# Optimization experiments

Measured on AMD Instinct MI355X. Metric: run time of the kernel, lower is better.

## Reference

```python
import jax, jax.numpy as jnp
import numpy as np

D_NODE = 256
D_PAIR = 128
C = 32
H = 8
LN_EPS = 1e-5


def layer_norm(x, g, b):
    m = jnp.mean(x, axis=-1, keepdims=True)
    v = jnp.mean(jnp.square(x - m), axis=-1, keepdims=True)
    return (x - m) * jax.lax.rsqrt(v + LN_EPS) * g + b


def self_attention(x, mask, wq, wk, wv, wg, bg, wo, bo=None, bias=None):
    # x: [B, S, R, d], mask: [B, S, R]
    B, S, R, _ = x.shape
    scale = 1.0 / np.sqrt(C)
    q = (jnp.einsum('bsrd,ed->bsre', x, wq) * scale).reshape(B, S, R, H, C)
    k = jnp.einsum('bsrd,ed->bsre', x, wk).reshape(B, S, R, H, C)
    v = jnp.einsum('bsrd,ed->bsre', x, wv).reshape(B, S, R, H, C)
    logits = jnp.einsum('bsqhc,bskhc->bshqk', q, k)
    logits = logits + (1e9 * (mask - 1.0))[:, :, None, None, :]
    if bias is not None:
        logits = logits + bias[:, None]  # [B,1,H,R,R]
    a = jax.nn.softmax(logits, axis=-1)
    o = jnp.einsum('bshqk,bskhc->bsqhc', a, v).reshape(B, S, R, H * C)
    g = jax.nn.sigmoid(jnp.einsum('bsrd,ed->bsre', x, wg) + bg)
    out = jnp.einsum('bsre,de->bsrd', o * g, wo)
    if bo is not None:
        out = out + bo
    return out


def setup_inputs() -> dict:
    key = jax.random.key(0)
    ks = jax.random.split(key, 24)
    B, S, R = 1, 128, 256
    d, dp, hc, dff = D_NODE, D_PAIR, H * C, 4 * D_NODE
    std = 0.02
    inp = {
        'node': jax.random.normal(ks[0], (B, S, R, d), jnp.float32),
        'pair': jax.random.normal(ks[1], (B, R, R, dp), jnp.float32),
        'node_mask': jnp.ones((B, S, R), jnp.float32),
        # row attention (pair-biased)
        'row_ln_m_g': jnp.ones((d,), jnp.float32),
        'row_ln_m_b': jnp.zeros((d,), jnp.float32),
        'row_ln_z_g': jnp.ones((dp,), jnp.float32),
        'row_ln_z_b': jnp.zeros((dp,), jnp.float32),
        'row_b_w': jax.random.normal(ks[2], (H, dp), jnp.float32) / np.sqrt(dp),
        'row_wq': jax.random.normal(ks[3], (hc, d), jnp.float32) * std,
        'row_wk': jax.random.normal(ks[4], (hc, d), jnp.float32) * std,
        'row_wv': jax.random.normal(ks[5], (hc, d), jnp.float32) * std,
        'row_wg': jax.random.normal(ks[6], (hc, d), jnp.float32) * std,
        'row_bg': jnp.ones((hc,), jnp.float32),
        'row_wo': jax.random.normal(ks[7], (d, hc), jnp.float32) * std,
        'row_out_bias': jnp.zeros((d,), jnp.float32),
        # column attention
        'col_ln_g': jnp.ones((d,), jnp.float32),
        'col_ln_b': jnp.zeros((d,), jnp.float32),
        'col_wq': jax.random.normal(ks[8], (hc, d), jnp.float32) * std,
        'col_wk': jax.random.normal(ks[9], (hc, d), jnp.float32) * std,
        'col_wv': jax.random.normal(ks[10], (hc, d), jnp.float32) * std,
        'col_wg': jax.random.normal(ks[11], (hc, d), jnp.float32) * std,
        'col_bg': jnp.ones((hc,), jnp.float32),
        'col_wo': jax.random.normal(ks[12], (d, hc), jnp.float32) * std,
        'col_bo': jnp.zeros((d,), jnp.float32),
        # transition
        'tr_ln_g': jnp.ones((d,), jnp.float32),
        'tr_ln_b': jnp.zeros((d,), jnp.float32),
        'tr_w1': jax.random.normal(ks[13], (dff, d), jnp.float32) * std,
        'tr_b1': jnp.zeros((dff,), jnp.float32),
        'tr_w2': jax.random.normal(ks[14], (d, dff), jnp.float32) * std,
        'tr_b2': jnp.zeros((d,), jnp.float32),
    }
    return inp


def reference(node, pair, node_mask,
              row_ln_m_g, row_ln_m_b, row_ln_z_g, row_ln_z_b, row_b_w,
              row_wq, row_wk, row_wv, row_wg, row_bg, row_wo, row_out_bias,
              col_ln_g, col_ln_b, col_wq, col_wk, col_wv, col_wg, col_bg,
              col_wo, col_bo, tr_ln_g, tr_ln_b, tr_w1, tr_b1, tr_w2, tr_b2):
    # --- MSA row attention with pair bias ---
    M = layer_norm(node, row_ln_m_g, row_ln_m_b)
    Z = layer_norm(pair, row_ln_z_g, row_ln_z_b)
    b = jnp.einsum('bqkd,hd->bhqk', Z, row_b_w)  # pair bias [B,H,R,R]
    attn = self_attention(M, node_mask, row_wq, row_wk, row_wv,
                          row_wg, row_bg, row_wo, bo=None, bias=b)
    # bias_dropout_add in eval mode: residual + attn + fused out bias
    node = node + attn + row_out_bias
    # --- MSA column attention ---
    Mt = jnp.swapaxes(node, 1, 2)            # [B,R,S,d]
    Mn = layer_norm(Mt, col_ln_g, col_ln_b)
    mask_t = jnp.swapaxes(node_mask, 1, 2)   # [B,R,S]
    attn_c = self_attention(Mn, mask_t, col_wq, col_wk, col_wv,
                            col_wg, col_bg, col_wo, bo=col_bo)
    node = node + jnp.swapaxes(attn_c, 1, 2)
    # --- MSA transition ---
    t = layer_norm(node, tr_ln_g, tr_ln_b)
    t = jax.nn.relu(jnp.einsum('bsrd,ed->bsre', t, tr_w1) + tr_b1)
    node = node + (jnp.einsum('bsre,de->bsrd', t, tr_w2) + tr_b2)
    return node
```

## Files before the change

kernel.cpp:

```cpp
#include <hip/hip_runtime.h>
#include <math.h>

#define S 128
#define R 256
#define DMODEL 256
#define H 8
#define CDIM 32
#define HC 256
#define DFF 1024
#define NROWS (S*R)
#define NPAIR (R*R)
#define LN_EPS 1e-5f
#define LOG2E 1.4426950408889634f
#define M32 ((size_t)NROWS * 32)

typedef unsigned short u16;
typedef __attribute__((ext_vector_type(8))) short bf16x8;
typedef __attribute__((ext_vector_type(4))) float f32x4;
typedef __attribute__((ext_vector_type(16))) float f32x16;

__device__ __forceinline__ u16 f2bf(float x) {
  unsigned u = __float_as_uint(x);
  u = (u + 0x7fffu + ((u >> 16) & 1u)) >> 16;
  return (u16)u;
}
__device__ __forceinline__ float bf2f(u16 x) {
  return __uint_as_float(((unsigned)x) << 16);
}
__device__ __forceinline__ unsigned cvt_pk(float a, float b) {
  unsigned r;
  asm("v_cvt_pk_bf16_f32 %0, %1, %2" : "=v"(r) : "v"(a), "v"(b));
  return r;
}
__device__ __forceinline__ void pl32swap(unsigned &a, unsigned &b) {
  asm("v_permlane32_swap_b32 %0, %1" : "+v"(a), "+v"(b));
}
__device__ __forceinline__ bf16x8 mk_frag(unsigned a, unsigned b, unsigned c, unsigned d) {
  uint4 t = make_uint4(a, b, c, d);
  return __builtin_bit_cast(bf16x8, t);
}

__device__ __forceinline__ void gload_lds16(const u16* g, u16* l) {
  __builtin_amdgcn_global_load_lds(
      (const __attribute__((address_space(1))) unsigned int*)g,
      (__attribute__((address_space(3))) unsigned int*)l, 16, 0, 0);
}

struct CvtArgs {
  const float* src[12];
  int off[12];
  int n[12];
  float scale[12];
};

__global__ __launch_bounds__(256) void cvt_w_kernel(CvtArgs a, u16* __restrict__ dst) {
  int sg = blockIdx.y;
  int i = (blockIdx.x * 256 + threadIdx.x) * 4;
  if (i >= a.n[sg]) return;
  float4 v = *(const float4*)(a.src[sg] + i);
  float sc = a.scale[sg];
  uint2 o;
  o.x = cvt_pk(v.x * sc, v.y * sc);
  o.y = cvt_pk(v.z * sc, v.w * sc);
  *(uint2*)(dst + a.off[sg] + i) = o;
}

__global__ __launch_bounds__(256) void ln256_kernel(
    const void* __restrict__ in, u16* __restrict__ out,
    const float* __restrict__ gamma, const float* __restrict__ beta,
    int tmode, int inbf)
{
  int wid = threadIdx.x >> 6, lane = threadIdx.x & 63;
  int m = blockIdx.x * 4 + wid;
  int inrow = m;
  if (tmode) { int r = m >> 7, s = m & 127; inrow = s * R + r; }
  float4 x;
  if (inbf) {
    ushort4 u = *(const ushort4*)((const u16*)in + (size_t)inrow * DMODEL + lane * 4);
    x.x = bf2f(u.x); x.y = bf2f(u.y); x.z = bf2f(u.z); x.w = bf2f(u.w);
  } else {
    x = *(const float4*)((const float*)in + (size_t)inrow * DMODEL + lane * 4);
  }
  float sum = x.x + x.y + x.z + x.w;
  float sq  = x.x*x.x + x.y*x.y + x.z*x.z + x.w*x.w;
  #pragma unroll
  for (int off = 32; off; off >>= 1) {
    sum += __shfl_xor(sum, off);
    sq  += __shfl_xor(sq, off);
  }
  float mean = sum * (1.0f/256.0f);
  float var  = sq  * (1.0f/256.0f) - mean*mean;
  float rstd = rsqrtf(var + LN_EPS);
  float4 g = *(const float4*)(gamma + lane*4);
  float4 b = *(const float4*)(beta  + lane*4);
  uint2 o;
  o.x = cvt_pk((x.x-mean)*rstd*g.x + b.x, (x.y-mean)*rstd*g.y + b.y);
  o.y = cvt_pk((x.z-mean)*rstd*g.z + b.z, (x.w-mean)*rstd*g.w + b.w);
  *(uint2*)(out + (size_t)m * DMODEL + lane*4) = o;
}

__global__ __launch_bounds__(256) void pair_bias_kernel(
    const float* __restrict__ pair, const float* __restrict__ gamma,
    const float* __restrict__ beta, const float* __restrict__ bw,
    u16* __restrict__ bias)
{
  int wid = threadIdx.x >> 6, lane = threadIdx.x & 63;
  int p = blockIdx.x * 4 + wid;
  float2 x = *(const float2*)(pair + (size_t)p * 128 + lane*2);
  float sum = x.x + x.y, sq = x.x*x.x + x.y*x.y;
  #pragma unroll
  for (int off = 32; off; off >>= 1) {
    sum += __shfl_xor(sum, off);
    sq  += __shfl_xor(sq, off);
  }
  float mean = sum * (1.0f/128.0f);
  float rstd = rsqrtf(sq*(1.0f/128.0f) - mean*mean + LN_EPS);
  float z0 = (x.x-mean)*rstd*gamma[lane*2]   + beta[lane*2];
  float z1 = (x.y-mean)*rstd*gamma[lane*2+1] + beta[lane*2+1];
  float a0 = z0*bw[0*128+lane*2] + z1*bw[0*128+lane*2+1];
  float a1 = z0*bw[1*128+lane*2] + z1*bw[1*128+lane*2+1];
  float a2 = z0*bw[2*128+lane*2] + z1*bw[2*128+lane*2+1];
  float a3 = z0*bw[3*128+lane*2] + z1*bw[3*128+lane*2+1];
  float a4 = z0*bw[4*128+lane*2] + z1*bw[4*128+lane*2+1];
  float a5 = z0*bw[5*128+lane*2] + z1*bw[5*128+lane*2+1];
  float a6 = z0*bw[6*128+lane*2] + z1*bw[6*128+lane*2+1];
  float a7 = z0*bw[7*128+lane*2] + z1*bw[7*128+lane*2+1];
  #pragma unroll
  for (int off = 32; off; off >>= 1) {
    a0 += __shfl_xor(a0, off); a1 += __shfl_xor(a1, off);
    a2 += __shfl_xor(a2, off); a3 += __shfl_xor(a3, off);
    a4 += __shfl_xor(a4, off); a5 += __shfl_xor(a5, off);
    a6 += __shfl_xor(a6, off); a7 += __shfl_xor(a7, off);
  }
  float v = a0;
  v = (lane==1)?a1:v; v = (lane==2)?a2:v; v = (lane==3)?a3:v;
  v = (lane==4)?a4:v; v = (lane==5)?a5:v; v = (lane==6)?a6:v; v = (lane==7)?a7:v;
  if (lane < 8) {
    int q = p >> 8, k = p & 255;
    int kt = k >> 5, qt = q >> 5, c31 = q & 31;
    int kk = k & 31;
    int hi2 = (kk >> 2) & 1;
    int j = (kk & 3) | ((kk >> 3) << 2);
    size_t addr = ((((size_t)lane*8 + kt)*8 + qt)*2 + hi2)*512 + (size_t)c31*16 + j;
    bias[addr] = f2bf(v * LOG2E);
  }
}

template<int AM>
__global__ __launch_bounds__(512, 2) void gemm_8ph(
    const u16* __restrict__ A, const u16* __restrict__ W,
    void* __restrict__ Cout, int N, int K,
    int mode, const float* __restrict__ bias, const float* __restrict__ res)
{
  __shared__ u16 lds[2][AM+2][128*64];
  int t = threadIdx.x, lane = t & 63, wv = t >> 6;
  int g16 = (lane >> 4) & 3, l16 = lane & 15;
  int wm = wv >> 2, wn = wv & 3;
  int lrow = lane >> 3, lchunk = lane & 7;

  int gx = gridDim.x;
  int nwg = gx * gridDim.y;
  int p = blockIdx.y * gx + blockIdx.x;
  int cpx = nwg >> 3;
  int lg = (p & 7) * cpx + (p >> 3);
  int bn = (lg % gx) * 256;
  int bm = (lg / gx) * (AM * 128);

  int srcc = (lchunk ^ lrow) << 3;
  int ch0  = (g16 ^ (l16 & 7)) << 3;
  int rdoff = l16 * 64 + ch0;
  const int wnh = AM + (wn >> 1);
  const int wnr = (wn & 1) * 4096;

  f32x4 acc[AM*4][4];
  #pragma unroll
  for (int i = 0; i < AM*4; ++i)
    #pragma unroll
    for (int j = 0; j < 4; ++j) acc[i][j] = (f32x4){0.f,0.f,0.f,0.f};

  const int nkt = K >> 6;

#define STG_HALF(buf_, h_, base_, row0_, kc_) do { \
    gload_lds16(base_ + (size_t)((row0_) + (wv*2+0)*8 + lrow) * K + (kc_) + srcc, \
                &lds[buf_][h_][(wv*2+0)*512 + lane*8]); \
    gload_lds16(base_ + (size_t)((row0_) + (wv*2+1)*8 + lrow) * K + (kc_) + srcc, \
                &lds[buf_][h_][(wv*2+1)*512 + lane*8]); \
  } while(0)
#define STG_A(buf_, kc_) do { STG_HALF(buf_,0,A,bm,kc_); \
    if (AM==2) STG_HALF(buf_,1,A,bm+128,kc_); } while(0)
#define STG_B(buf_, kc_) do { STG_HALF(buf_,AM,W,bn,kc_); STG_HALF(buf_,AM+1,W,bn+128,kc_); } while(0)

  int buf = 0;
  STG_A(0, 0); STG_B(0, 0);
  for (int kt = 0; kt < nkt; ++kt) {
    int kc = kt << 6;
    if (kt + 1 < nkt) {
      STG_A(buf^1, kc + 64);
      if (AM == 2) asm volatile("s_waitcnt vmcnt(4)" ::: "memory");
      else         asm volatile("s_waitcnt vmcnt(2)" ::: "memory");
    } else {
      asm volatile("s_waitcnt vmcnt(0)" ::: "memory");
    }
    __builtin_amdgcn_s_barrier();
    asm volatile("" ::: "memory");
    if (kt + 1 < nkt) STG_B(buf^1, kc + 64);

    const u16* Abase = (AM==2) ? &lds[buf][wm][0] : &lds[buf][0][wm*4096];
    const u16* Wbase = &lds[buf][wnh][wnr];
    bf16x8 wf[4][2];
    #pragma unroll
    for (int nf = 0; nf < 4; ++nf) {
      wf[nf][0] = *(const bf16x8*)(Wbase + nf*1024 + rdoff);
      wf[nf][1] = *(const bf16x8*)(Wbase + nf*1024 + (rdoff ^ 32));
    }
    __builtin_amdgcn_s_setprio(1);
    #pragma unroll
    for (int mf = 0; mf < AM*4; ++mf) {
      bf16x8 a0 = *(const bf16x8*)(Abase + mf*1024 + rdoff);
      bf16x8 a1 = *(const bf16x8*)(Abase + mf*1024 + (rdoff ^ 32));
      #pragma unroll
      for (int nf = 0; nf < 4; ++nf) {
        acc[mf][nf] = __builtin_amdgcn_mfma_f32_16x16x32_bf16(wf[nf][0], a0, acc[mf][nf], 0, 0, 0);
        acc[mf][nf] = __builtin_amdgcn_mfma_f32_16x16x32_bf16(wf[nf][1], a1, acc[mf][nf], 0, 0, 0);
      }
    }
    __builtin_amdgcn_s_setprio(0);
    asm volatile("" ::: "memory");
    __builtin_amdgcn_s_barrier();
    buf ^= 1;
  }
#undef STG_A
#undef STG_B
#undef STG_HALF

  const u16* resb = (const u16*)res;
  int rowb = bm + wm*(AM*64) + l16;
  int colb = bn + wn*64 + (g16 << 2);
  #pragma unroll
  for (int mf = 0; mf < AM*4; ++mf) {
    int row = rowb + mf*16;
    #pragma unroll
    for (int nf = 0; nf < 4; ++nf) {
      int col0 = colb + nf*16;
      f32x4 v = acc[mf][nf];
      if (mode == 6) {
        if (col0 >= 768) {
          float4 b4 = *(const float4*)(bias + col0 - 768);
          v[0] = 1.0f/(1.0f+__expf(-(v[0]+b4.x)));
          v[1] = 1.0f/(1.0f+__expf(-(v[1]+b4.y)));
          v[2] = 1.0f/(1.0f+__expf(-(v[2]+b4.z)));
          v[3] = 1.0f/(1.0f+__expf(-(v[3]+b4.w)));
        }
        uint2 o; o.x = cvt_pk(v[0], v[1]); o.y = cvt_pk(v[2], v[3]);
        size_t i2 = (size_t)(col0 >> 5) * M32 + (size_t)row*32 + (col0 & 31);
        *(uint2*)((u16*)Cout + i2) = o;
      } else if (mode == 3) {
        float4 b4 = *(const float4*)(bias + col0);
        uint2 o;
        o.x = cvt_pk(fmaxf(v[0]+b4.x, 0.f), fmaxf(v[1]+b4.y, 0.f));
        o.y = cvt_pk(fmaxf(v[2]+b4.z, 0.f), fmaxf(v[3]+b4.w, 0.f));
        *(uint2*)((u16*)Cout + (size_t)row*N + col0) = o;
      } else if (mode == 4) {
        size_t i2 = (size_t)row*N + col0;
        float4 r4 = *(const float4*)(res + i2);
        float4 b4 = *(const float4*)(bias + col0);
        float4 o = make_float4(v[0]+r4.x+b4.x, v[1]+r4.y+b4.y,
                               v[2]+r4.z+b4.z, v[3]+r4.w+b4.w);
        *(float4*)((float*)Cout + i2) = o;
      } else if (mode == 5) {
        int rr = row >> 7, ss = row & 127;
        size_t i2 = ((size_t)ss*R + rr)*(size_t)N + col0;
        float4 r4 = *(const float4*)(res + i2);
        float4 b4 = *(const float4*)(bias + col0);
        float4 o = make_float4(v[0]+r4.x+b4.x, v[1]+r4.y+b4.y,
                               v[2]+r4.z+b4.z, v[3]+r4.w+b4.w);
        *(float4*)((float*)Cout + i2) = o;
      } else if (mode == 7) {
        size_t i2 = (size_t)row*N + col0;
        float4 r4 = *(const float4*)(res + i2);
        float4 b4 = *(const float4*)(bias + col0);
        uint2 o;
        o.x = cvt_pk(v[0]+r4.x+b4.x, v[1]+r4.y+b4.y);
        o.y = cvt_pk(v[2]+r4.z+b4.z, v[3]+r4.w+b4.w);
        *(uint2*)((u16*)Cout + i2) = o;
      } else if (mode == 8) {
        int rr = row >> 7, ss = row & 127;
        size_t i2 = ((size_t)ss*R + rr)*(size_t)N + col0;
        ushort4 r4 = *(const ushort4*)(resb + i2);
        float4 b4 = *(const float4*)(bias + col0);
        uint2 o;
        o.x = cvt_pk(v[0]+bf2f(r4.x)+b4.x, v[1]+bf2f(r4.y)+b4.y);
        o.y = cvt_pk(v[2]+bf2f(r4.z)+b4.z, v[3]+bf2f(r4.w)+b4.w);
        *(uint2*)((u16*)Cout + i2) = o;
      } else if (mode == 9) {
        size_t i2 = (size_t)row*N + col0;
        ushort4 r4 = *(const ushort4*)(resb + i2);
        float4 b4 = *(const float4*)(bias + col0);
        float4 o = make_float4(v[0]+bf2f(r4.x)+b4.x, v[1]+bf2f(r4.y)+b4.y,
                               v[2]+bf2f(r4.z)+b4.z, v[3]+bf2f(r4.w)+b4.w);
        *(float4*)((float*)Cout + i2) = o;
      } else if (mode == 2) {
        float4 b4 = *(const float4*)(bias + col0);
        uint2 o;
        o.x = cvt_pk(1.0f/(1.0f+__expf(-(v[0]+b4.x))),
                     1.0f/(1.0f+__expf(-(v[1]+b4.y))));
        o.y = cvt_pk(1.0f/(1.0f+__expf(-(v[2]+b4.z))),
                     1.0f/(1.0f+__expf(-(v[3]+b4.w))));
        *(uint2*)((u16*)Cout + (size_t)row*N + col0) = o;
      } else {
        uint2 o; o.x = cvt_pk(v[0], v[1]); o.y = cvt_pk(v[2], v[3]);
        *(uint2*)((u16*)Cout + (size_t)row*N + col0) = o;
      }
    }
  }
}

template<bool RM>
__device__ __forceinline__ void softmax_pack(
    const f32x16 &sac, const float* __restrict__ lmbp,
    bf16x8 bf0, bf16x8 bf1, int kb, int hi,
    float &lsum, bf16x8 &pf0, bf16x8 &pf1)
{
  float p[16];
  #pragma unroll
  for (int rq = 0; rq < 4; ++rq) {
    int k0 = kb + 8*rq + 4*hi;
    float4 lm4 = *(const float4*)&lmbp[k0];
    float b0 = lm4.x, b1 = lm4.y, b2 = lm4.z, b3 = lm4.w;
    if (RM) {
      if (rq < 2) {
        b0 += bf2f((u16)bf0[4*rq+0]); b1 += bf2f((u16)bf0[4*rq+1]);
        b2 += bf2f((u16)bf0[4*rq+2]); b3 += bf2f((u16)bf0[4*rq+3]);
      } else {
        b0 += bf2f((u16)bf1[4*rq-8+0]); b1 += bf2f((u16)bf1[4*rq-8+1]);
        b2 += bf2f((u16)bf1[4*rq-8+2]); b3 += bf2f((u16)bf1[4*rq-8+3]);
      }
    }
    p[4*rq+0] = exp2f(sac[4*rq+0] + b0);
    p[4*rq+1] = exp2f(sac[4*rq+1] + b1);
    p[4*rq+2] = exp2f(sac[4*rq+2] + b2);
    p[4*rq+3] = exp2f(sac[4*rq+3] + b3);
    lsum += (p[4*rq+0] + p[4*rq+1]) + (p[4*rq+2] + p[4*rq+3]);
  }
  unsigned u0 = cvt_pk(p[0],  p[1]),  u1 = cvt_pk(p[2],  p[3]);
  unsigned u2 = cvt_pk(p[4],  p[5]),  u3 = cvt_pk(p[6],  p[7]);
  unsigned u4 = cvt_pk(p[8],  p[9]),  u5 = cvt_pk(p[10], p[11]);
  unsigned u6 = cvt_pk(p[12], p[13]), u7 = cvt_pk(p[14], p[15]);
  pl32swap(u0, u2); pl32swap(u1, u3);
  pl32swap(u4, u6); pl32swap(u5, u7);
  pf0 = mk_frag(u0, u1, u2, u3);
  pf1 = mk_frag(u4, u5, u6, u7);
}

template<int NKEY, int HPB, bool ROWMODE>
__global__ __launch_bounds__(512, 2) void attn_mfma(
    const u16* __restrict__ QKVG, const u16* __restrict__ biasF,
    const float* __restrict__ mask, u16* __restrict__ og)
{
  __shared__ __align__(16) u16 Vt[HPB][32][NKEY + 8];
  __shared__ float lmb[NKEY];
  constexpr int NKV = NKEY / 32;
  constexpr int WPH = 8 / HPB;
  int b = blockIdx.y;
  int t = threadIdx.x, lane = t & 63, w = t >> 6;
  int c31 = lane & 31, hi = lane >> 5;
  int lh = w / WPH, wtile = w % WPH;
  int hh = blockIdx.x * HPB + lh;

  size_t rbase = (size_t)b * NKEY * 32;
  const u16* Qp = QKVG + (size_t)hh * M32 + rbase;
  const u16* Kp = QKVG + (size_t)(8 + hh) * M32 + rbase;
  const u16* Gp = QKVG + (size_t)(24 + hh) * M32 + rbase;

  for (int i = t; i < HPB*NKEY*4; i += 512) {
    int c0 = (i & 3) * 8;
    int key = (i >> 2) & (NKEY - 1);
    int sh = (i >> 2) / NKEY;
    const u16* Vs = QKVG + (size_t)(16 + blockIdx.x*HPB + sh) * M32 + rbase;
    bf16x8 v8 = *(const bf16x8*)(Vs + (size_t)key*32 + c0);
    #pragma unroll
    for (int j = 0; j < 8; ++j) Vt[sh][c0+j][key] = (u16)v8[j];
  }
  for (int i = t; i < NKEY; i += 512)
    lmb[i] = 1.4426950e9f * ((ROWMODE ? mask[b*R + i] : mask[i*R + b]) - 1.0f);
  __syncthreads();

  int qA = wtile*64 + c31, qB = qA + 32;
  int qtA = wtile*2, qtB = wtile*2 + 1;
  bf16x8 qfA0 = *(const bf16x8*)(Qp + (size_t)qA*32 + hi*8);
  bf16x8 qfA1 = *(const bf16x8*)(Qp + (size_t)qA*32 + 16 + hi*8);
  bf16x8 qfB0 = *(const bf16x8*)(Qp + (size_t)qB*32 + hi*8);
  bf16x8 qfB1 = *(const bf16x8*)(Qp + (size_t)qB*32 + 16 + hi*8);

  f32x16 oA = (f32x16)(0.0f), oB = (f32x16)(0.0f);
  float lsA = 0.f, lsB = 0.f;

#define LOADK(d0_, d1_, g_) do { \
    const u16* kr_ = Kp + ((size_t)((g_)*32) + c31)*32 + hi*8; \
    d0_ = *(const bf16x8*)kr_; d1_ = *(const bf16x8*)(kr_ + 16); \
  } while(0)

#define GROUP_BODY(g_, k0_, k1_) do { \
    int kb_ = (g_) * 32; \
    bf16x8 bA0{}, bA1{}, bB0{}, bB1{}; \
    if (ROWMODE) { \
      const u16* bpA_ = biasF + ((((size_t)hh*8 + (g_))*8 + qtA)*2 + hi)*512 + (size_t)c31*16; \
      bA0 = *(const bf16x8*)bpA_; bA1 = *(const bf16x8*)(bpA_ + 8); \
    } \
    __builtin_amdgcn_s_setprio(1); \
    f32x16 sacA_ = __builtin_amdgcn_mfma_f32_32x32x16_bf16(k0_, qfA0, (f32x16)(0.0f), 0, 0, 0); \
    sacA_ = __builtin_amdgcn_mfma_f32_32x32x16_bf16(k1_, qfA1, sacA_, 0, 0, 0); \
    __builtin_amdgcn_s_setprio(0); \
    bf16x8 va0_ = *(const bf16x8*)&Vt[lh][c31][kb_ + hi*8]; \
    bf16x8 va1_ = *(const bf16x8*)&Vt[lh][c31][kb_ + 16 + hi*8]; \
    bf16x8 pf0_, pf1_; \
    softmax_pack<ROWMODE>(sacA_, lmb, bA0, bA1, kb_, hi, lsA, pf0_, pf1_); \
    __builtin_amdgcn_s_setprio(1); \
    oA = __builtin_amdgcn_mfma_f32_32x32x16_bf16(va0_, pf0_, oA, 0, 0, 0); \
    oA = __builtin_amdgcn_mfma_f32_32x32x16_bf16(va1_, pf1_, oA, 0, 0, 0); \
    __builtin_amdgcn_s_setprio(0); \
    if (ROWMODE) { \
      const u16* bpB_ = biasF + ((((size_t)hh*8 + (g_))*8 + qtB)*2 + hi)*512 + (size_t)c31*16; \
      bB0 = *(const bf16x8*)bpB_; bB1 = *(const bf16x8*)(bpB_ + 8); \
    } \
    __builtin_amdgcn_s_setprio(1); \
    f32x16 sacB_ = __builtin_amdgcn_mfma_f32_32x32x16_bf16(k0_, qfB0, (f32x16)(0.0f), 0, 0, 0); \
    sacB_ = __builtin_amdgcn_mfma_f32_32x32x16_bf16(k1_, qfB1, sacB_, 0, 0, 0); \
    __builtin_amdgcn_s_setprio(0); \
    softmax_pack<ROWMODE>(sacB_, lmb, bB0, bB1, kb_, hi, lsB, pf0_, pf1_); \
    __builtin_amdgcn_s_setprio(1); \
    oB = __builtin_amdgcn_mfma_f32_32x32x16_bf16(va0_, pf0_, oB, 0, 0, 0); \
    oB = __builtin_amdgcn_mfma_f32_32x32x16_bf16(va1_, pf1_, oB, 0, 0, 0); \
    __builtin_amdgcn_s_setprio(0); \
  } while(0)

  bf16x8 ke0{}, ke1{}, ko0{}, ko1{};
  LOADK(ke0, ke1, 0);
  LOADK(ko0, ko1, 1);
  for (int g = 0; g < NKV; g += 2) {
    bf16x8 c0 = ke0, c1 = ke1;
    if (g + 2 < NKV) LOADK(ke0, ke1, g + 2);
    GROUP_BODY(g, c0, c1);
    bf16x8 d0 = ko0, d1 = ko1;
    if (g + 3 < NKV) LOADK(ko0, ko1, g + 3);
    GROUP_BODY(g + 1, d0, d1);
  }
#undef GROUP_BODY
#undef LOADK

  lsA += __shfl_xor(lsA, 32);
  lsB += __shfl_xor(lsB, 32);
  float invA = 1.0f / lsA, invB = 1.0f / lsB;

  size_t baseO = (size_t)b * NKEY * 256 + (size_t)hh * 32;
  #pragma unroll
  for (int tile = 0; tile < 2; ++tile) {
    int q = (tile == 0) ? qA : qB;
    float inv = (tile == 0) ? invA : invB;
    const f32x16 &oo = (tile == 0) ? oA : oB;
    u16* op = og + baseO + (size_t)q * 256;
    const u16* gp = Gp + (size_t)q * 32;
    #pragma unroll
    for (int rq = 0; rq < 4; ++rq) {
      int c0 = 8*rq + 4*hi;
      ushort4 g4 = *(const ushort4*)(gp + c0);
      float f0 = oo[4*rq+0] * inv * bf2f(g4.x);
      float f1 = oo[4*rq+1] * inv * bf2f(g4.y);
      float f2 = oo[4*rq+2] * inv * bf2f(g4.z);
      float f3 = oo[4*rq+3] * inv * bf2f(g4.w);
      uint2 o2; o2.x = cvt_pk(f0, f1); o2.y = cvt_pk(f2, f3);
      *(uint2*)(op + c0) = o2;
    }
  }
}

extern "C" void kernel_launch(void* const* d_in, const int* in_sizes, int n_in,
                              void* d_out, int out_size, void* d_ws, size_t ws_size,
                              hipStream_t stream)
{
  const float* node         = (const float*)d_in[0];
  const float* pair         = (const float*)d_in[1];
  const float* node_mask    = (const float*)d_in[2];
  const float* row_ln_m_g   = (const float*)d_in[3];
  const float* row_ln_m_b   = (const float*)d_in[4];
  const float* row_ln_z_g   = (const float*)d_in[5];
  const float* row_ln_z_b   = (const float*)d_in[6];
  const float* row_b_w      = (const float*)d_in[7];
  const float* row_wq       = (const float*)d_in[8];
  const float* row_wk       = (const float*)d_in[9];
  const float* row_wv       = (const float*)d_in[10];
  const float* row_wg       = (const float*)d_in[11];
  const float* row_bg       = (const float*)d_in[12];
  const float* row_wo       = (const float*)d_in[13];
  const float* row_out_bias = (const float*)d_in[14];
  const float* col_ln_g     = (const float*)d_in[15];
  const float* col_ln_b     = (const float*)d_in[16];
  const float* col_wq       = (const float*)d_in[17];
  const float* col_wk       = (const float*)d_in[18];
  const float* col_wv       = (const float*)d_in[19];
  const float* col_wg       = (const float*)d_in[20];
  const float* col_bg       = (const float*)d_in[21];
  const float* col_wo       = (const float*)d_in[22];
  const float* col_bo       = (const float*)d_in[23];
  const float* tr_ln_g      = (const float*)d_in[24];
  const float* tr_ln_b      = (const float*)d_in[25];
  const float* tr_w1        = (const float*)d_in[26];
  const float* tr_b1        = (const float*)d_in[27];
  const float* tr_w2        = (const float*)d_in[28];
  const float* tr_b2        = (const float*)d_in[29];

  float* out = (float*)d_out;
  char* ws8 = (char*)d_ws;
  const size_t MB = 1ull << 20;
  u16*   A     = (u16*)(ws8);
  u16*   QKVG  = (u16*)(ws8 + 16*MB);
  u16*   Ob    = (u16*)(ws8 + 80*MB);
  u16*   DbF   = (u16*)(ws8 + 96*MB);
  u16*   N1    = (u16*)(ws8 + 100*MB);
  u16*   N2    = (u16*)(ws8 + 116*MB);
  u16*   Wb    = (u16*)(ws8 + 132*MB);
  u16*   T1    = QKVG;

  const float qs = 0.17677669529663687f;

  u16* Wrqkvg = Wb + 0;
  u16* Wro    = Wb + 262144;
  u16* Wcqkvg = Wb + 327680;
  u16* Wco    = Wb + 589824;
  u16* W1w    = Wb + 655360;
  u16* W2w    = Wb + 917504;

  CvtArgs ca;
  const float* srcs[12] = {row_wq,row_wk,row_wv,row_wg,row_wo,
                           col_wq,col_wk,col_wv,col_wg,col_wo,tr_w1,tr_w2};
  int offs[12] = {0,65536,131072,196608,262144,327680,393216,458752,524288,589824,655360,917504};
  int ns[12]   = {65536,65536,65536,65536,65536,65536,65536,65536,65536,65536,262144,262144};
  for (int i = 0; i < 12; ++i) {
    ca.src[i] = srcs[i]; ca.off[i] = offs[i]; ca.n[i] = ns[i];
    ca.scale[i] = (i == 0 || i == 5) ? qs * LOG2E : 1.0f;
  }
  cvt_w_kernel<<<dim3(256,12), 256, 0, stream>>>(ca, Wb);

  dim3 gq(4, 128);
  dim3 go(1, 256);

  ln256_kernel<<<8192, 256, 0, stream>>>(node, A, row_ln_m_g, row_ln_m_b, 0, 0);
  pair_bias_kernel<<<16384, 256, 0, stream>>>(pair, row_ln_z_g, row_ln_z_b, row_b_w, DbF);
  gemm_8ph<2><<<gq, 512, 0, stream>>>(A, Wrqkvg, QKVG, 1024, 256, 6, row_bg, nullptr);
  attn_mfma<256,2,true><<<dim3(4,128), 512, 0, stream>>>(QKVG, DbF, node_mask, Ob);
  gemm_8ph<1><<<go, 512, 0, stream>>>(Ob, Wro, N1, 256, 256, 7, row_out_bias, node);

  ln256_kernel<<<8192, 256, 0, stream>>>(N1, A, col_ln_g, col_ln_b, 1, 1);
  gemm_8ph<2><<<gq, 512, 0, stream>>>(A, Wcqkvg, QKVG, 1024, 256, 6, col_bg, nullptr);
  attn_mfma<128,4,false><<<dim3(2,256), 512, 0, stream>>>(QKVG, nullptr, node_mask, Ob);
  gemm_8ph<1><<<go, 512, 0, stream>>>(Ob, Wco, N2, 256, 256, 8, col_bo, (const float*)N1);

  ln256_kernel<<<8192, 256, 0, stream>>>(N2, A, tr_ln_g, tr_ln_b, 0, 1);
  gemm_8ph<2><<<gq, 512, 0, stream>>>(A, W1w, T1, 1024, 256, 3, tr_b1, nullptr);
  gemm_8ph<1><<<go, 512, 0, stream>>>(T1, W2w, out, 256, 1024, 9, tr_b2, (const float*)N2);
}
```

Measured before the change: 345.8 us.

## Switch GEMM to triple-buffered K=32 LDS pipeline with prefetch depth two

Rewrites the GEMM main loop to use three LDS buffers of 32-wide K tiles instead of two 64-wide tiles, issuing global-to-LDS loads two iterations ahead. The aim is to hide global load latency better and reduce LDS footprint per stage, possibly improving occupancy. In exchange it doubles the number of loop iterations and barriers per K, and changes the swizzle pattern, which could add bank conflicts or overhead.

```diff
diff --git a/kernel.cpp b/kernel.cpp
--- a/kernel.cpp
+++ b/kernel.cpp
@@ -152,11 +152,10 @@
     void* __restrict__ Cout, int N, int K,
     int mode, const float* __restrict__ bias, const float* __restrict__ res)
 {
-  __shared__ u16 lds[2][AM+2][128*64];
+  __shared__ u16 lds[3][AM+2][128*32];
   int t = threadIdx.x, lane = t & 63, wv = t >> 6;
   int g16 = (lane >> 4) & 3, l16 = lane & 15;
   int wm = wv >> 2, wn = wv & 3;
-  int lrow = lane >> 3, lchunk = lane & 7;
 
   int gx = gridDim.x;
   int nwg = gx * gridDim.y;
@@ -166,11 +165,12 @@
   int bn = (lg % gx) * 256;
   int bm = (lg / gx) * (AM * 128);
 
-  int srcc = (lchunk ^ lrow) << 3;
-  int ch0  = (g16 ^ (l16 & 7)) << 3;
-  int rdoff = l16 * 64 + ch0;
+  int sr = t >> 2;
+  int swz8 = ((t & 3) ^ ((sr >> 1) & 3)) << 3;
+  int rdch = (g16 ^ ((l16 >> 1) & 3)) << 3;
+  int rdoff = l16 * 32 + rdch;
   const int wnh = AM + (wn >> 1);
-  const int wnr = (wn & 1) * 4096;
+  const int wnr = (wn & 1) * 2048;
 
   f32x4 acc[AM*4][4];
   #pragma unroll
@@ -178,60 +178,50 @@
     #pragma unroll
     for (int j = 0; j < 4; ++j) acc[i][j] = (f32x4){0.f,0.f,0.f,0.f};
 
-  const int nkt = K >> 6;
-
-#define STG_HALF(buf_, h_, base_, row0_, kc_) do { \
-    gload_lds16(base_ + (size_t)((row0_) + (wv*2+0)*8 + lrow) * K + (kc_) + srcc, \
-                &lds[buf_][h_][(wv*2+0)*512 + lane*8]); \
-    gload_lds16(base_ + (size_t)((row0_) + (wv*2+1)*8 + lrow) * K + (kc_) + srcc, \
-                &lds[buf_][h_][(wv*2+1)*512 + lane*8]); \
+  const int nkt = K >> 5;
+
+#define STAGE(buf_, kc_) do { \
+    gload_lds16(A + (size_t)(bm + sr) * K + (kc_) + swz8, &lds[buf_][0][t*8]); \
+    if (AM == 2) \
+      gload_lds16(A + (size_t)(bm + 128 + sr) * K + (kc_) + swz8, &lds[buf_][1][t*8]); \
+    gload_lds16(W + (size_t)(bn + sr) * K + (kc_) + swz8, &lds[buf_][AM][t*8]); \
+    gload_lds16(W + (size_t)(bn + 128 + sr) * K + (kc_) + swz8, &lds[buf_][AM+1][t*8]); \
   } while(0)
-#define STG_A(buf_, kc_) do { STG_HALF(buf_,0,A,bm,kc_); \
-    if (AM==2) STG_HALF(buf_,1,A,bm+128,kc_); } while(0)
-#define STG_B(buf_, kc_) do { STG_HALF(buf_,AM,W,bn,kc_); STG_HALF(buf_,AM+1,W,bn+128,kc_); } while(0)
-
-  int buf = 0;
-  STG_A(0, 0); STG_B(0, 0);
+
+  STAGE(0, 0);
+  STAGE(1, 32);
   for (int kt = 0; kt < nkt; ++kt) {
-    int kc = kt << 6;
-    if (kt + 1 < nkt) {
-      STG_A(buf^1, kc + 64);
+    if (kt + 2 < nkt) {
+      STAGE((kt + 2) % 3, (kt + 2) * 32);
+      if (AM == 2) asm volatile("s_waitcnt vmcnt(8)" ::: "memory");
+      else         asm volatile("s_waitcnt vmcnt(6)" ::: "memory");
+    } else if (kt + 1 < nkt) {
       if (AM == 2) asm volatile("s_waitcnt vmcnt(4)" ::: "memory");
-      else         asm volatile("s_waitcnt vmcnt(2)" ::: "memory");
+      else         asm volatile("s_waitcnt vmcnt(3)" ::: "memory");
     } else {
       asm volatile("s_waitcnt vmcnt(0)" ::: "memory");
     }
     __builtin_amdgcn_s_barrier();
-    asm volatile("" ::: "memory");
-    if (kt + 1 < nkt) STG_B(buf^1, kc + 64);
-
-    const u16* Abase = (AM==2) ? &lds[buf][wm][0] : &lds[buf][0][wm*4096];
+    int buf = kt % 3;
+    const u16* Abase = (AM == 2) ? &lds[buf][wm][0] : &lds[buf][0][wm*2048];
     const u16* Wbase = &lds[buf][wnh][wnr];
-    bf16x8 wf[4][2];
+    bf16x8 wf[4];
     #pragma unroll
-    for (int nf = 0; nf < 4; ++nf) {
-      wf[nf][0] = *(const bf16x8*)(Wbase + nf*1024 + rdoff);
-      wf[nf][1] = *(const bf16x8*)(Wbase + nf*1024 + (rdoff ^ 32));
-    }
+    for (int nf = 0; nf < 4; ++nf)
+      wf[nf] = *(const bf16x8*)(Wbase + nf*512 + rdoff);
     __builtin_amdgcn_s_setprio(1);
     #pragma unroll
     for (int mf = 0; mf < AM*4; ++mf) {
-      bf16x8 a0 = *(const bf16x8*)(Abase + mf*1024 + rdoff);
-      bf16x8 a1 = *(const bf16x8*)(Abase + mf*1024 + (rdoff ^ 32));
+      bf16x8 a0 = *(const bf16x8*)(Abase + mf*512 + rdoff);
       #pragma unroll
-      for (int nf = 0; nf < 4; ++nf) {
-        acc[mf][nf] = __builtin_amdgcn_mfma_f32_16x16x32_bf16(wf[nf][0], a0, acc[mf][nf], 0, 0, 0);
-        acc[mf][nf] = __builtin_amdgcn_mfma_f32_16x16x32_bf16(wf[nf][1], a1, acc[mf][nf], 0, 0, 0);
-      }
+      for (int nf = 0; nf < 4; ++nf)
+        acc[mf][nf] = __builtin_amdgcn_mfma_f32_16x16x32_bf16(wf[nf], a0, acc[mf][nf], 0, 0, 0);
     }
     __builtin_amdgcn_s_setprio(0);
     asm volatile("" ::: "memory");
     __builtin_amdgcn_s_barrier();
-    buf ^= 1;
-  }
-#undef STG_A
-#undef STG_B
-#undef STG_HALF
+  }
+#undef STAGE
 
   const u16* resb = (const u16*)res;
   int rowb = bm + wm*(AM*64) + l16;
```

Result: slower. 352.8 us (+2.0%).
